# Kernel optimization log

Hardware: AMD Instinct MI355X
Metric: run time of the kernel (lower is better)

The kernel has to match this reference:

```python
import jax, jax.numpy as jnp
import numpy as np

B = 2; L = 5000; C_IN = 12
D_MODEL = 512; D_STATE = 64; D_CONV = 4
D_INNER = 2 * D_MODEL            # mamba expand=2
DT_RANK = (D_MODEL + 15) // 16   # ceil(d_model/16) = 32
NUM_CLASSES = 8


def setup_inputs() -> dict:
    ks = jax.random.split(jax.random.key(0), 16)
    f32 = jnp.float32
    n = lambda k, s, sc: jax.random.normal(k, s, f32) * sc
    return {
        "x": jax.random.normal(ks[0], (B, C_IN, L), f32),
        # 1x1 convs stored as (out_ch, in_ch)
        "w_init": n(ks[1], (D_MODEL, C_IN), 0.1),
        "w_final": n(ks[2], (C_IN, D_MODEL), 0.05),
        # Mamba params
        "w_in": n(ks[3], (2 * D_INNER, D_MODEL), 0.02),
        "conv_w": n(ks[4], (D_INNER, D_CONV), 0.2),   # depthwise taps
        "conv_b": jnp.zeros((D_INNER,), f32),
        "w_xproj": n(ks[5], (DT_RANK + 2 * D_STATE, D_INNER), 0.02),
        "w_dt": n(ks[6], (D_INNER, DT_RANK), 0.1),
        "b_dt": jnp.full((D_INNER,), -4.6, f32),      # softplus(-4.6) ~ 0.01
        "A_log": jnp.log(jnp.broadcast_to(jnp.arange(1, D_STATE + 1, dtype=f32), (D_INNER, D_STATE))),
        "D": jnp.ones((D_INNER,), f32),
        "w_out": n(ks[7], (D_MODEL, D_INNER), 0.02),
        # MLP head
        "w_fc1": n(ks[8], (512, C_IN * L), 0.004),
        "b_fc1": jnp.zeros((512,), f32),
        "w_fc2": n(ks[9], (256, 512), 0.04),
        "b_fc2": jnp.zeros((256,), f32),
        "w_fc3": n(ks[10], (64, 256), 0.06),
        "b_fc3": jnp.zeros((64,), f32),
        "w_fc4": n(ks[11], (NUM_CLASSES, 64), 0.1),
        "b_fc4": jnp.zeros((NUM_CLASSES,), f32),
    }


def _mamba(u, w_in, conv_w, conv_b, w_xproj, w_dt, b_dt, A_log, D, w_out):
    # u: (B, L, d_model)
    xz = jnp.einsum('bld,ed->ble', u, w_in)            # (B, L, 2*d_inner)
    xi, z = jnp.split(xz, 2, axis=-1)
    # causal depthwise conv, kernel width D_CONV (torch pads d_conv-1, takes [:L])
    xpad = jnp.pad(xi, ((0, 0), (D_CONV - 1, 0), (0, 0)))
    xc = conv_b + sum(xpad[:, k:k + L, :] * conv_w[:, k] for k in range(D_CONV))
    xc = jax.nn.silu(xc)                               # (B, L, d_inner)
    x_dbl = jnp.einsum('bld,ed->ble', xc, w_xproj)
    dt_lo = x_dbl[..., :DT_RANK]
    Bm = x_dbl[..., DT_RANK:DT_RANK + D_STATE]         # (B, L, d_state)
    Cm = x_dbl[..., DT_RANK + D_STATE:]                # (B, L, d_state)
    dt = jax.nn.softplus(jnp.einsum('blr,dr->bld', dt_lo, w_dt) + b_dt)
    A = -jnp.exp(A_log)                                # (d_inner, d_state)

    def step(h, inp):
        dt_t, B_t, C_t, u_t = inp                      # (B,di) (B,ds) (B,ds) (B,di)
        dA = jnp.exp(dt_t[:, :, None] * A)             # (B, d_inner, d_state)
        h = dA * h + (dt_t * u_t)[:, :, None] * B_t[:, None, :]
        y_t = jnp.einsum('bds,bs->bd', h, C_t)
        return h, y_t

    h0 = jnp.zeros((u.shape[0], D_INNER, D_STATE), u.dtype)
    xs = (dt.transpose(1, 0, 2), Bm.transpose(1, 0, 2),
          Cm.transpose(1, 0, 2), xc.transpose(1, 0, 2))
    _, ys = jax.lax.scan(jax.checkpoint(step), h0, xs)  # ys: (L, B, d_inner)
    y = ys.transpose(1, 0, 2) + xc * D
    y = y * jax.nn.silu(z)
    return jnp.einsum('bld,md->blm', y, w_out)          # (B, L, d_model)


def reference(x, w_init, w_final, w_in, conv_w, conv_b, w_xproj, w_dt, b_dt,
              A_log, D, w_out, w_fc1, b_fc1, w_fc2, b_fc2, w_fc3, b_fc3,
              w_fc4, b_fc4):
    # initial 1x1 conv + transpose -> (B, L, d_model)
    h = jnp.einsum('bcl,dc->bld', x, w_init)
    m = _mamba(h, w_in, conv_w, conv_b, w_xproj, w_dt, b_dt, A_log, D, w_out)
    m = jax.nn.selu(m)                                  # AlphaDropout: identity in eval
    o = jnp.einsum('bld,cd->bcl', m, w_final)           # final 1x1 conv -> (B, 12, L)
    f = o.reshape(o.shape[0], -1)                       # (B, 60000)
    f = f @ w_fc1.T + b_fc1
    f = f @ w_fc2.T + b_fc2
    f = f @ w_fc3.T + b_fc3
    return f @ w_fc4.T + b_fc4                          # (B, num_classes)
```

## Files before the change

### kernel.cpp

```cpp
#include <hip/hip_runtime.h>

#define BB 2
#define LL 5000
#define DM 512
#define DI 1024
#define DSz 64
#define DRr 32
#define NXx 160
#define ML (BB*LL)
#define NC 25
#define LC 200

typedef short bf16x8 __attribute__((ext_vector_type(8)));
typedef float f32x4 __attribute__((ext_vector_type(4)));

__device__ __forceinline__ float siluf(float x) { return x / (1.0f + __expf(-x)); }
__device__ __forceinline__ float softplusf(float x) { return fmaxf(x, 0.0f) + log1pf(__expf(-fabsf(x))); }
__device__ __forceinline__ float seluf(float x) {
  const float sc = 1.0507009873554805f, al = 1.6732632423543772f;
  return x > 0.0f ? sc * x : sc * al * (__expf(x) - 1.0f);
}
__device__ __forceinline__ void bfsplit(float v, ushort& hi, ushort& lo) {
  unsigned u = __float_as_uint(v);
  unsigned h = (u + 0x7fffu + ((u >> 16) & 1u)) >> 16;
  hi = (ushort)h;
  float l = v - __uint_as_float(h << 16);
  unsigned ul = __float_as_uint(l);
  lo = (ushort)((ul + 0x7fffu + ((ul >> 16) & 1u)) >> 16);
}
__device__ __forceinline__ float bfrecon(ushort hi, ushort lo) {
  return __uint_as_float((unsigned)hi << 16) + __uint_as_float((unsigned)lo << 16);
}

__global__ __launch_bounds__(256) void cvt_split_kernel(
    const float* __restrict__ src, ushort* __restrict__ hi, ushort* __restrict__ lo, int n)
{
  int i = (blockIdx.x * 256 + threadIdx.x) * 4;
  if (i >= n) return;
  float4 v = *reinterpret_cast<const float4*>(src + i);
  ushort h0, l0, h1, l1, h2, l2, h3, l3;
  bfsplit(v.x, h0, l0); bfsplit(v.y, h1, l1);
  bfsplit(v.z, h2, l2); bfsplit(v.w, h3, l3);
  *reinterpret_cast<ushort4*>(hi + i) = make_ushort4(h0, h1, h2, h3);
  *reinterpret_cast<ushort4*>(lo + i) = make_ushort4(l0, l1, l2, l3);
}

__global__ __launch_bounds__(512) void init_h_split_kernel(
    const float* __restrict__ x, const float* __restrict__ w_init,
    ushort* __restrict__ hh, ushort* __restrict__ hl)
{
  int il = blockIdx.x;
  int b = il / LL, l = il - b * LL;
  int dd = threadIdx.x;
  const float* xp = x + (size_t)b * 12 * LL + l;
  float acc = 0.f;
#pragma unroll
  for (int c = 0; c < 12; ++c) acc = fmaf(xp[(size_t)c * LL], w_init[dd * 12 + c], acc);
  ushort h, lo; bfsplit(acc, h, lo);
  hh[(size_t)il * DM + dd] = h;
  hl[(size_t)il * DM + dd] = lo;
}

template<int ACT, int SPLITN>
__global__ __launch_bounds__(256) void gemm_mfma(
    const ushort* __restrict__ Ahi, const ushort* __restrict__ Alo,
    const ushort* __restrict__ Bhi, const ushort* __restrict__ Blo,
    float* __restrict__ C, float* __restrict__ C2, int M, int N, int K)
{
  __shared__ ushort lds[4][128][40];
  int tid = threadIdx.x;
  int i0 = blockIdx.x * 128, j0 = blockIdx.y * 128;
  int l = tid & 63, wid = tid >> 6;
  int wm = (wid >> 1) * 64, wn = (wid & 1) * 64;
  int lr = l & 15, lk = (l >> 4) * 8;
  int sr = tid >> 1, kb = (tid & 1) * 16;

  f32x4 acc[4][4];
#pragma unroll
  for (int m = 0; m < 4; ++m)
#pragma unroll
    for (int n = 0; n < 4; ++n) acc[m][n] = (f32x4){0.f, 0.f, 0.f, 0.f};

  const uint4 z4 = make_uint4(0u, 0u, 0u, 0u);
  for (int k0 = 0; k0 < K; k0 += 32) {
    __syncthreads();
    {
      int gi = i0 + sr, gj = j0 + sr;
      size_t aoff = (size_t)gi * K + k0 + kb;
      size_t boff = (size_t)gj * K + k0 + kb;
      uint4 a0 = z4, a1 = z4, b0 = z4, b1 = z4, c0 = z4, c1 = z4, d0 = z4, d1 = z4;
      if (gi < M) {
        a0 = *reinterpret_cast<const uint4*>(Ahi + aoff);
        a1 = *reinterpret_cast<const uint4*>(Ahi + aoff + 8);
        b0 = *reinterpret_cast<const uint4*>(Alo + aoff);
        b1 = *reinterpret_cast<const uint4*>(Alo + aoff + 8);
      }
      if (gj < N) {
        c0 = *reinterpret_cast<const uint4*>(Bhi + boff);
        c1 = *reinterpret_cast<const uint4*>(Bhi + boff + 8);
        d0 = *reinterpret_cast<const uint4*>(Blo + boff);
        d1 = *reinterpret_cast<const uint4*>(Blo + boff + 8);
      }
      *reinterpret_cast<uint4*>(&lds[0][sr][kb]) = a0;
      *reinterpret_cast<uint4*>(&lds[0][sr][kb + 8]) = a1;
      *reinterpret_cast<uint4*>(&lds[1][sr][kb]) = b0;
      *reinterpret_cast<uint4*>(&lds[1][sr][kb + 8]) = b1;
      *reinterpret_cast<uint4*>(&lds[2][sr][kb]) = c0;
      *reinterpret_cast<uint4*>(&lds[2][sr][kb + 8]) = c1;
      *reinterpret_cast<uint4*>(&lds[3][sr][kb]) = d0;
      *reinterpret_cast<uint4*>(&lds[3][sr][kb + 8]) = d1;
    }
    __syncthreads();
    bf16x8 ah[4], av[4], bh[4], bv[4];
#pragma unroll
    for (int m = 0; m < 4; ++m) {
      ah[m] = *reinterpret_cast<const bf16x8*>(&lds[0][wm + m * 16 + lr][lk]);
      av[m] = *reinterpret_cast<const bf16x8*>(&lds[1][wm + m * 16 + lr][lk]);
    }
#pragma unroll
    for (int n = 0; n < 4; ++n) {
      bh[n] = *reinterpret_cast<const bf16x8*>(&lds[2][wn + n * 16 + lr][lk]);
      bv[n] = *reinterpret_cast<const bf16x8*>(&lds[3][wn + n * 16 + lr][lk]);
    }
#pragma unroll
    for (int m = 0; m < 4; ++m)
#pragma unroll
      for (int n = 0; n < 4; ++n) {
        acc[m][n] = __builtin_amdgcn_mfma_f32_16x16x32_bf16(ah[m], bh[n], acc[m][n], 0, 0, 0);
        acc[m][n] = __builtin_amdgcn_mfma_f32_16x16x32_bf16(av[m], bh[n], acc[m][n], 0, 0, 0);
        acc[m][n] = __builtin_amdgcn_mfma_f32_16x16x32_bf16(ah[m], bv[n], acc[m][n], 0, 0, 0);
      }
  }

#pragma unroll
  for (int m = 0; m < 4; ++m) {
    int r0 = i0 + wm + m * 16 + (l >> 4) * 4;
#pragma unroll
    for (int n = 0; n < 4; ++n) {
      int gc = j0 + wn + n * 16 + lr;
      if (gc >= N) continue;
#pragma unroll
      for (int q = 0; q < 4; ++q) {
        int gi = r0 + q;
        if (gi >= M) continue;
        float r = acc[m][n][q];
        if (ACT == 1) r = seluf(r);
        if (SPLITN) {
          int half = N >> 1;
          if (gc < half) C[(size_t)gi * half + gc] = r;
          else C2[(size_t)gi * half + (gc - half)] = r;
        } else {
          C[(size_t)gi * N + gc] = r;
        }
      }
    }
  }
}

template<int ACT>
__global__ __launch_bounds__(256) void gemm_nt(
    const float* __restrict__ A, const float* __restrict__ Bw,
    const float* __restrict__ bias, float* __restrict__ C,
    int M, int N, int K, int lda, int ldb)
{
  __shared__ float As[16][132];
  __shared__ float Bs[16][132];
  int tid = threadIdx.x;
  int i0 = blockIdx.x * 128, j0 = blockIdx.y * 128;
  int tx = tid & 15, ty = tid >> 4;
  int lr = tid >> 2, lc = tid & 3;
  float acc[8][8];
#pragma unroll
  for (int u = 0; u < 8; ++u)
#pragma unroll
    for (int v = 0; v < 8; ++v) acc[u][v] = 0.f;

  for (int k0 = 0; k0 < K; k0 += 16) {
    __syncthreads();
#pragma unroll
    for (int hh = 0; hh < 2; ++hh) {
      int row = lr + 64 * hh;
      int gi = i0 + row;
      float4 va = make_float4(0.f, 0.f, 0.f, 0.f);
      if (gi < M) va = *reinterpret_cast<const float4*>(A + (size_t)gi * lda + k0 + lc * 4);
      As[lc * 4 + 0][row] = va.x; As[lc * 4 + 1][row] = va.y;
      As[lc * 4 + 2][row] = va.z; As[lc * 4 + 3][row] = va.w;
      int gj = j0 + row;
      float4 vb = make_float4(0.f, 0.f, 0.f, 0.f);
      if (gj < N) vb = *reinterpret_cast<const float4*>(Bw + (size_t)gj * ldb + k0 + lc * 4);
      Bs[lc * 4 + 0][row] = vb.x; Bs[lc * 4 + 1][row] = vb.y;
      Bs[lc * 4 + 2][row] = vb.z; Bs[lc * 4 + 3][row] = vb.w;
    }
    __syncthreads();
#pragma unroll
    for (int kk = 0; kk < 16; ++kk) {
      float4 a0 = *reinterpret_cast<const float4*>(&As[kk][8 * ty]);
      float4 a1 = *reinterpret_cast<const float4*>(&As[kk][8 * ty + 4]);
      float4 b0 = *reinterpret_cast<const float4*>(&Bs[kk][8 * tx]);
      float4 b1 = *reinterpret_cast<const float4*>(&Bs[kk][8 * tx + 4]);
      float av[8] = {a0.x, a0.y, a0.z, a0.w, a1.x, a1.y, a1.z, a1.w};
      float bv[8] = {b0.x, b0.y, b0.z, b0.w, b1.x, b1.y, b1.z, b1.w};
#pragma unroll
      for (int u = 0; u < 8; ++u)
#pragma unroll
        for (int v = 0; v < 8; ++v) acc[u][v] = fmaf(av[u], bv[v], acc[u][v]);
    }
  }

#pragma unroll
  for (int u = 0; u < 8; ++u) {
    int gi = i0 + 8 * ty + u;
    if (gi >= M) continue;
#pragma unroll
    for (int v = 0; v < 8; ++v) {
      int gj = j0 + 8 * tx + v;
      if (gj >= N) continue;
      float r = acc[u][v];
      if (bias) r += bias[gj];
      if (ACT == 1) r = seluf(r);
      if (ACT == 2) r = softplusf(r);
      C[(size_t)gi * N + gj] = r;
    }
  }
}

__global__ __launch_bounds__(256) void conv_silu_split_kernel(
    const float* __restrict__ xi, const float* __restrict__ cw,
    const float* __restrict__ cb, ushort* __restrict__ xch, ushort* __restrict__ xcl)
{
  int il = blockIdx.x;
  int l = il % LL;
  int d = blockIdx.y * 256 + threadIdx.x;
  float acc = cb[d];
  if (l >= 3) acc = fmaf(xi[(size_t)(il - 3) * DI + d], cw[d * 4 + 0], acc);
  if (l >= 2) acc = fmaf(xi[(size_t)(il - 2) * DI + d], cw[d * 4 + 1], acc);
  if (l >= 1) acc = fmaf(xi[(size_t)(il - 1) * DI + d], cw[d * 4 + 2], acc);
  acc = fmaf(xi[(size_t)il * DI + d], cw[d * 4 + 3], acc);
  float v = siluf(acc);
  ushort h, lo; bfsplit(v, h, lo);
  xch[(size_t)il * DI + d] = h;
  xcl[(size_t)il * DI + d] = lo;
}

template<int ACT>
__global__ __launch_bounds__(256) void transpose_k(
    const float* __restrict__ in, float* __restrict__ out,
    int R, int Cc, int ldin, long long bstr)
{
  __shared__ float tile[32][33];
  const float* ip = in + (size_t)blockIdx.z * bstr;
  float* op = out + (size_t)blockIdx.z * bstr;
  int r0 = blockIdx.x * 32, c0 = blockIdx.y * 32;
  int tx = threadIdx.x, ty2 = threadIdx.y;
#pragma unroll
  for (int i = ty2; i < 32; i += 8) {
    int r = r0 + i, c = c0 + tx;
    if (r < R && c < Cc) {
      float v = ip[(size_t)r * ldin + c];
      if (ACT == 1) v = siluf(v);
      tile[i][tx] = v;
    }
  }
  __syncthreads();
#pragma unroll
  for (int i = ty2; i < 32; i += 8) {
    int c = c0 + i, r = r0 + tx;
    if (r < R && c < Cc) op[(size_t)c * R + r] = tile[tx][i];
  }
}

__global__ __launch_bounds__(256) void transpose_recon_k(
    const ushort* __restrict__ inhi, const ushort* __restrict__ inlo,
    float* __restrict__ out, int R, int Cc, int ldin, long long bstr)
{
  __shared__ float tile[32][33];
  const ushort* iph = inhi + (size_t)blockIdx.z * bstr;
  const ushort* ipl = inlo + (size_t)blockIdx.z * bstr;
  float* op = out + (size_t)blockIdx.z * bstr;
  int r0 = blockIdx.x * 32, c0 = blockIdx.y * 32;
  int tx = threadIdx.x, ty2 = threadIdx.y;
#pragma unroll
  for (int i = ty2; i < 32; i += 8) {
    int r = r0 + i, c = c0 + tx;
    if (r < R && c < Cc) {
      size_t idx = (size_t)r * ldin + c;
      tile[i][tx] = bfrecon(iph[idx], ipl[idx]);
    }
  }
  __syncthreads();
#pragma unroll
  for (int i = ty2; i < 32; i += 8) {
    int c = c0 + i, r = r0 + tx;
    if (r < R && c < Cc) op[(size_t)c * R + r] = tile[tx][i];
  }
}

__global__ __launch_bounds__(256) void transpose_split_k(
    const float* __restrict__ in, ushort* __restrict__ outhi, ushort* __restrict__ outlo,
    int R, int Cc, int ldin, long long bstr)
{
  __shared__ float tile[32][33];
  const float* ip = in + (size_t)blockIdx.z * bstr;
  ushort* oph = outhi + (size_t)blockIdx.z * bstr;
  ushort* opl = outlo + (size_t)blockIdx.z * bstr;
  int r0 = blockIdx.x * 32, c0 = blockIdx.y * 32;
  int tx = threadIdx.x, ty2 = threadIdx.y;
#pragma unroll
  for (int i = ty2; i < 32; i += 8) {
    int r = r0 + i, c = c0 + tx;
    if (r < R && c < Cc) tile[i][tx] = ip[(size_t)r * ldin + c];
  }
  __syncthreads();
#pragma unroll
  for (int i = ty2; i < 32; i += 8) {
    int c = c0 + i, r = r0 + tx;
    if (r < R && c < Cc) {
      ushort h, lo; bfsplit(tile[tx][i], h, lo);
      size_t idx = (size_t)c * R + r;
      oph[idx] = h; opl[idx] = lo;
    }
  }
}

__global__ __launch_bounds__(256) void scan_part_kernel(
    const float* __restrict__ dtT, const float* __restrict__ uT,
    const float* __restrict__ xdbl, const float* __restrict__ A_log,
    float2* __restrict__ part)
{
  int task = (blockIdx.x * 256 + threadIdx.x) >> 4;
  int j = threadIdx.x & 15;
  int bd = task / NC, c = task - bd * NC;
  int b = bd >> 10, d = bd & (DI - 1);
  float4 Al = *reinterpret_cast<const float4*>(A_log + d * DSz + 4 * j);
  float Ac0 = -__expf(Al.x), Ac1 = -__expf(Al.y), Ac2 = -__expf(Al.z), Ac3 = -__expf(Al.w);
  size_t base = (size_t)bd * LL + c * LC;
  const float* pdt = dtT + base;
  const float* pu = uT + base;
  const float4* pB4 = reinterpret_cast<const float4*>(
      xdbl + ((size_t)b * LL + c * LC) * NXx + DRr) + j;
  float h0 = 0.f, h1 = 0.f, h2 = 0.f, h3 = 0.f;
  float ap0 = 1.f, ap1 = 1.f, ap2 = 1.f, ap3 = 1.f;
#pragma unroll 4
  for (int t = 0; t < LC; ++t) {
    float dtv = pdt[t];
    float u = pu[t];
    float4 Bv = pB4[0]; pB4 += NXx / 4;
    float du = dtv * u;
    float a0 = __expf(dtv * Ac0); h0 = fmaf(a0, h0, du * Bv.x); ap0 *= a0;
    float a1 = __expf(dtv * Ac1); h1 = fmaf(a1, h1, du * Bv.y); ap1 *= a1;
    float a2 = __expf(dtv * Ac2); h2 = fmaf(a2, h2, du * Bv.z); ap2 *= a2;
    float a3 = __expf(dtv * Ac3); h3 = fmaf(a3, h3, du * Bv.w); ap3 *= a3;
  }
  float4* pw = reinterpret_cast<float4*>(part + (size_t)task * DSz + 4 * j);
  pw[0] = make_float4(ap0, h0, ap1, h1);
  pw[1] = make_float4(ap2, h2, ap3, h3);
}

__global__ __launch_bounds__(256) void scan_y_kernel(
    const float* __restrict__ dtT, const float* __restrict__ uT,
    const float* __restrict__ szT, const float* __restrict__ xdbl,
    const float* __restrict__ A_log, const float* __restrict__ Dv,
    const float2* __restrict__ part, float* __restrict__ yT)
{
  int task = (blockIdx.x * 256 + threadIdx.x) >> 4;
  int j = threadIdx.x & 15;
  int bd = task / NC, c = task - bd * NC;
  int b = bd >> 10, d = bd & (DI - 1);
  float4 Al = *reinterpret_cast<const float4*>(A_log + d * DSz + 4 * j);
  float Ac0 = -__expf(Al.x), Ac1 = -__expf(Al.y), Ac2 = -__expf(Al.z), Ac3 = -__expf(Al.w);
  float Dd = Dv[d];

  float h0 = 0.f, h1 = 0.f, h2 = 0.f, h3 = 0.f;
  const float4* pp = reinterpret_cast<const float4*>(part + (size_t)bd * NC * DSz) + 2 * j;
  for (int p = 0; p < c; ++p) {
    float4 v01 = pp[(size_t)p * (DSz / 2)];
    float4 v23 = pp[(size_t)p * (DSz / 2) + 1];
    h0 = fmaf(v01.x, h0, v01.y);
    h1 = fmaf(v01.z, h1, v01.w);
    h2 = fmaf(v23.x, h2, v23.y);
    h3 = fmaf(v23.z, h3, v23.w);
  }

  size_t base = (size_t)bd * LL + c * LC;
  const float* pdt = dtT + base;
  const float* pu = uT + base;
  const float* psz = szT + base;
  float* py = yT + base;
  const float4* pB4 = reinterpret_cast<const float4*>(
      xdbl + ((size_t)b * LL + c * LC) * NXx + DRr) + j;

  for (int t0 = 0; t0 < LC; t0 += 8) {
    float pr[8], uu[8], szv[8];
#pragma unroll
    for (int i = 0; i < 8; ++i) {
      float dtv = pdt[t0 + i];
      float u = pu[t0 + i];
      uu[i] = u;
      szv[i] = psz[t0 + i];
      float4 Bv = pB4[0];
      float4 Cv = pB4[DSz / 4];
      pB4 += NXx / 4;
      float du = dtv * u;
      float a0 = __expf(dtv * Ac0); h0 = fmaf(a0, h0, du * Bv.x);
      float a1 = __expf(dtv * Ac1); h1 = fmaf(a1, h1, du * Bv.y);
      float a2 = __expf(dtv * Ac2); h2 = fmaf(a2, h2, du * Bv.z);
      float a3 = __expf(dtv * Ac3); h3 = fmaf(a3, h3, du * Bv.w);
      float p = h0 * Cv.x;
      p = fmaf(h1, Cv.y, p);
      p = fmaf(h2, Cv.z, p);
      p = fmaf(h3, Cv.w, p);
      pr[i] = p;
    }
#pragma unroll
    for (int mm = 8; mm >= 1; mm >>= 1) {
#pragma unroll
      for (int i = 0; i < 8; ++i) pr[i] += __shfl_xor(pr[i], mm, 64);
    }
    if (j == 0) {
#pragma unroll
      for (int i = 0; i < 8; ++i) py[t0 + i] = fmaf(uu[i], Dd, pr[i]) * szv[i];
    }
  }
}

__global__ __launch_bounds__(256) void out_proj_kernel(
    const float* __restrict__ m, const float* __restrict__ wf, float* __restrict__ o)
{
  int row = blockIdx.x * 4 + (threadIdx.x >> 6);
  int lane = threadIdx.x & 63;
  int b = row / LL, l = row - b * LL;
  const float* mp = m + (size_t)row * DM;
  float p[12];
#pragma unroll
  for (int c = 0; c < 12; ++c) p[c] = 0.f;
  for (int j0 = 0; j0 < DM; j0 += 64) {
    float mv = mp[j0 + lane];
#pragma unroll
    for (int c = 0; c < 12; ++c) p[c] = fmaf(mv, wf[c * DM + j0 + lane], p[c]);
  }
#pragma unroll
  for (int c = 0; c < 12; ++c) {
    float v = p[c];
#pragma unroll
    for (int mm = 32; mm >= 1; mm >>= 1) v += __shfl_xor(v, mm, 64);
    if (lane == 0) o[(size_t)b * 60000 + c * LL + l] = v;
  }
}

__global__ __launch_bounds__(256) void fc1_kernel(
    const float* __restrict__ o, const float* __restrict__ w1,
    const float* __restrict__ b1, float* __restrict__ f1)
{
  int i = blockIdx.x;
  int tid = threadIdx.x;
  const float* wr = w1 + (size_t)i * 60000;
  float a0 = 0.f, a1 = 0.f;
  for (int idx = tid; idx < 60000; idx += 256) {
    float w = wr[idx];
    a0 = fmaf(o[idx], w, a0);
    a1 = fmaf(o[60000 + idx], w, a1);
  }
#pragma unroll
  for (int mm = 32; mm >= 1; mm >>= 1) { a0 += __shfl_xor(a0, mm, 64); a1 += __shfl_xor(a1, mm, 64); }
  __shared__ float r0[4], r1[4];
  int w4 = tid >> 6;
  if ((tid & 63) == 0) { r0[w4] = a0; r1[w4] = a1; }
  __syncthreads();
  if (tid == 0) {
    f1[i] = r0[0] + r0[1] + r0[2] + r0[3] + b1[i];
    f1[512 + i] = r1[0] + r1[1] + r1[2] + r1[3] + b1[i];
  }
}

__global__ __launch_bounds__(64) void fc2_kernel(
    const float* __restrict__ f1, const float* __restrict__ w2,
    const float* __restrict__ b2, float* __restrict__ f2)
{
  int i = blockIdx.x;
  int lane = threadIdx.x;
  const float* wr = w2 + (size_t)i * 512;
  float a0 = 0.f, a1 = 0.f;
  for (int k = lane; k < 512; k += 64) {
    float w = wr[k];
    a0 = fmaf(f1[k], w, a0);
    a1 = fmaf(f1[512 + k], w, a1);
  }
#pragma unroll
  for (int mm = 32; mm >= 1; mm >>= 1) { a0 += __shfl_xor(a0, mm, 64); a1 += __shfl_xor(a1, mm, 64); }
  if (lane == 0) { f2[i] = a0 + b2[i]; f2[256 + i] = a1 + b2[i]; }
}

__global__ __launch_bounds__(64) void fc34_kernel(
    const float* __restrict__ f2, const float* __restrict__ w3, const float* __restrict__ b3,
    const float* __restrict__ w4, const float* __restrict__ b4, float* __restrict__ outp)
{
  __shared__ float f3[128];
  int t = threadIdx.x;
  float a0 = 0.f, a1 = 0.f;
  for (int k = 0; k < 256; ++k) {
    float w = w3[t * 256 + k];
    a0 = fmaf(f2[k], w, a0);
    a1 = fmaf(f2[256 + k], w, a1);
  }
  f3[t] = a0 + b3[t];
  f3[64 + t] = a1 + b3[t];
  __syncthreads();
  if (t < 16) {
    int b = t >> 3, i = t & 7;
    float a = b4[i];
    for (int k = 0; k < 64; ++k) a = fmaf(f3[b * 64 + k], w4[i * 64 + k], a);
    outp[b * 8 + i] = a;
  }
}

extern "C" void kernel_launch(void* const* d_in, const int* in_sizes, int n_in,
                              void* d_out, int out_size, void* d_ws, size_t ws_size,
                              hipStream_t stream)
{
  const float* x       = (const float*)d_in[0];
  const float* w_init  = (const float*)d_in[1];
  const float* w_final = (const float*)d_in[2];
  const float* w_in    = (const float*)d_in[3];
  const float* conv_w  = (const float*)d_in[4];
  const float* conv_b  = (const float*)d_in[5];
  const float* w_xproj = (const float*)d_in[6];
  const float* w_dt    = (const float*)d_in[7];
  const float* b_dt    = (const float*)d_in[8];
  const float* A_log   = (const float*)d_in[9];
  const float* Dv      = (const float*)d_in[10];
  const float* w_out   = (const float*)d_in[11];
  const float* w_fc1   = (const float*)d_in[12];
  const float* b_fc1   = (const float*)d_in[13];
  const float* w_fc2   = (const float*)d_in[14];
  const float* b_fc2   = (const float*)d_in[15];
  const float* w_fc3   = (const float*)d_in[16];
  const float* b_fc3   = (const float*)d_in[17];
  const float* w_fc4   = (const float*)d_in[18];
  const float* b_fc4   = (const float*)d_in[19];

  float* ws = (float*)d_ws;
  const size_t S7 = 0;
  const size_t S1 = S7 + (size_t)ML * DM;
  const size_t S2 = S1 + (size_t)ML * DI;
  const size_t S3 = S2 + (size_t)ML * DI;
  const size_t S4 = S3 + (size_t)ML * DI;
  const size_t S5 = S4 + (size_t)ML * DI;
  const size_t S8 = S5 + (size_t)ML * DI;
  const size_t S9 = S8 + (size_t)ML * NXx;
  const size_t SF1 = S9 + 120000;
  const size_t SF2 = SF1 + 1024;

  ushort* h_hi = (ushort*)(ws + S7);
  ushort* h_lo = h_hi + (size_t)ML * DM;
  float*  xi   = ws + S1;
  float*  z    = ws + S2;
  ushort* xc_hi = (ushort*)(ws + S3);
  ushort* xc_lo = xc_hi + (size_t)ML * DI;
  float*  dtT  = ws + S4;
  float*  xcT  = ws + S5;
  float*  xdbl = ws + S8;
  float*  dt_l = ws + S1;
  float*  szT  = ws + S3;
  float2* part = (float2*)(ws + S2);
  float*  yT   = ws + S1;
  ushort* y_hi = (ushort*)(ws + S2);
  ushort* y_lo = y_hi + (size_t)ML * DI;
  float*  mbuf = ws + S7;
  float*  o    = ws + S9;
  float*  f1   = ws + SF1;
  float*  f2   = ws + SF2;

  ushort* wb    = (ushort*)(ws + S5);
  ushort* wi_hi = wb;
  ushort* wi_lo = wb + (size_t)2048 * 512;
  ushort* wx_hi = wb + (size_t)2 * 2048 * 512;
  ushort* wx_lo = wx_hi + (size_t)160 * 1024;
  ushort* wo_hi = wb;
  ushort* wo_lo = wb + (size_t)512 * 1024;

  const int GM = (ML + 127) / 128;
  dim3 tb(32, 8);

  cvt_split_kernel<<<1024, 256, 0, stream>>>(w_in, wi_hi, wi_lo, 2048 * 512);
  cvt_split_kernel<<<160, 256, 0, stream>>>(w_xproj, wx_hi, wx_lo, 160 * 1024);
  init_h_split_kernel<<<ML, 512, 0, stream>>>(x, w_init, h_hi, h_lo);
  gemm_mfma<0, 1><<<dim3(GM, 16), 256, 0, stream>>>(h_hi, h_lo, wi_hi, wi_lo, xi, z, ML, 2048, 512);
  conv_silu_split_kernel<<<dim3(ML, DI / 256), 256, 0, stream>>>(xi, conv_w, conv_b, xc_hi, xc_lo);
  gemm_mfma<0, 0><<<dim3(GM, 2), 256, 0, stream>>>(xc_hi, xc_lo, wx_hi, wx_lo, xdbl, nullptr, ML, NXx, 1024);
  gemm_nt<2><<<dim3(GM, DI / 128), 256, 0, stream>>>(xdbl, w_dt, b_dt, dt_l, ML, DI, DRr, NXx, DRr);
  transpose_k<0><<<dim3(157, 32, 2), tb, 0, stream>>>(dt_l, dtT, LL, DI, DI, (long long)LL * DI);
  transpose_recon_k<<<dim3(157, 32, 2), tb, 0, stream>>>(xc_hi, xc_lo, xcT, LL, DI, DI, (long long)LL * DI);
  transpose_k<1><<<dim3(157, 32, 2), tb, 0, stream>>>(z, szT, LL, DI, DI, (long long)LL * DI);
  scan_part_kernel<<<(BB * DI * NC) / 16, 256, 0, stream>>>(dtT, xcT, xdbl, A_log, part);
  scan_y_kernel<<<(BB * DI * NC) / 16, 256, 0, stream>>>(dtT, xcT, szT, xdbl, A_log, Dv, part, yT);
  cvt_split_kernel<<<512, 256, 0, stream>>>(w_out, wo_hi, wo_lo, 512 * 1024);
  transpose_split_k<<<dim3(32, 157, 2), tb, 0, stream>>>(yT, y_hi, y_lo, DI, LL, LL, (long long)LL * DI);
  gemm_mfma<1, 0><<<dim3(GM, 4), 256, 0, stream>>>(y_hi, y_lo, wo_hi, wo_lo, mbuf, nullptr, ML, DM, 1024);
  out_proj_kernel<<<ML / 4, 256, 0, stream>>>(mbuf, w_final, o);
  fc1_kernel<<<512, 256, 0, stream>>>(o, w_fc1, b_fc1, f1);
  fc2_kernel<<<256, 64, 0, stream>>>(f1, w_fc2, b_fc2, f2);
  fc34_kernel<<<1, 64, 0, stream>>>(f2, w_fc3, b_fc3, w_fc4, b_fc4, (float*)d_out);
}
```

Measured before the change: 1.251 ms.

## Fuse transposes into conv and dt-projection kernels, vectorize scan loads

```diff
diff --git a/kernel.cpp b/kernel.cpp
--- a/kernel.cpp
+++ b/kernel.cpp
@@ -27,9 +27,6 @@
   float l = v - __uint_as_float(h << 16);
   unsigned ul = __float_as_uint(l);
   lo = (ushort)((ul + 0x7fffu + ((ul >> 16) & 1u)) >> 16);
-}
-__device__ __forceinline__ float bfrecon(ushort hi, ushort lo) {
-  return __uint_as_float((unsigned)hi << 16) + __uint_as_float((unsigned)lo << 16);
 }
 
 __global__ __launch_bounds__(256) void cvt_split_kernel(
@@ -157,89 +154,76 @@
   }
 }
 
-template<int ACT>
-__global__ __launch_bounds__(256) void gemm_nt(
-    const float* __restrict__ A, const float* __restrict__ Bw,
-    const float* __restrict__ bias, float* __restrict__ C,
-    int M, int N, int K, int lda, int ldb)
-{
-  __shared__ float As[16][132];
-  __shared__ float Bs[16][132];
+__global__ __launch_bounds__(256) void conv_silu_split_t_kernel(
+    const float* __restrict__ xi, const float* __restrict__ cw,
+    const float* __restrict__ cb, ushort* __restrict__ xch, ushort* __restrict__ xcl,
+    float* __restrict__ xcT)
+{
+  __shared__ float tile[32][33];
+  int bz = blockIdx.z;
+  int l0 = blockIdx.x * 32, d0 = blockIdx.y * 32;
+  int tx = threadIdx.x, ty = threadIdx.y;
+  int d = d0 + tx;
+  float c0 = cw[d * 4 + 0], c1 = cw[d * 4 + 1], c2 = cw[d * 4 + 2], c3 = cw[d * 4 + 3];
+  float cbv = cb[d];
+#pragma unroll
+  for (int i = ty; i < 32; i += 8) {
+    int l = l0 + i;
+    if (l < LL) {
+      size_t il = (size_t)bz * LL + l;
+      float acc = cbv;
+      if (l >= 3) acc = fmaf(xi[(il - 3) * DI + d], c0, acc);
+      if (l >= 2) acc = fmaf(xi[(il - 2) * DI + d], c1, acc);
+      if (l >= 1) acc = fmaf(xi[(il - 1) * DI + d], c2, acc);
+      acc = fmaf(xi[il * DI + d], c3, acc);
+      float v = siluf(acc);
+      ushort h, lo; bfsplit(v, h, lo);
+      xch[il * DI + d] = h;
+      xcl[il * DI + d] = lo;
+      tile[i][tx] = v;
+    }
+  }
+  __syncthreads();
+#pragma unroll
+  for (int i = ty; i < 32; i += 8) {
+    int dd = d0 + i, l = l0 + tx;
+    if (l < LL) xcT[((size_t)bz * DI + dd) * LL + l] = tile[tx][i];
+  }
+}
+
+__global__ __launch_bounds__(256) void dtproj_t_kernel(
+    const float* __restrict__ xdbl, const float* __restrict__ w_dt,
+    const float* __restrict__ b_dt, float* __restrict__ dtT)
+{
+  __shared__ float wlds[16][32];
+  __shared__ float blds[16];
+  int bz = blockIdx.z;
+  int l0 = blockIdx.x * 64, d0 = blockIdx.y * 16;
   int tid = threadIdx.x;
-  int i0 = blockIdx.x * 128, j0 = blockIdx.y * 128;
-  int tx = tid & 15, ty = tid >> 4;
-  int lr = tid >> 2, lc = tid & 3;
-  float acc[8][8];
-#pragma unroll
-  for (int u = 0; u < 8; ++u)
-#pragma unroll
-    for (int v = 0; v < 8; ++v) acc[u][v] = 0.f;
-
-  for (int k0 = 0; k0 < K; k0 += 16) {
-    __syncthreads();
-#pragma unroll
-    for (int hh = 0; hh < 2; ++hh) {
-      int row = lr + 64 * hh;
-      int gi = i0 + row;
-      float4 va = make_float4(0.f, 0.f, 0.f, 0.f);
-      if (gi < M) va = *reinterpret_cast<const float4*>(A + (size_t)gi * lda + k0 + lc * 4);
-      As[lc * 4 + 0][row] = va.x; As[lc * 4 + 1][row] = va.y;
-      As[lc * 4 + 2][row] = va.z; As[lc * 4 + 3][row] = va.w;
-      int gj = j0 + row;
-      float4 vb = make_float4(0.f, 0.f, 0.f, 0.f);
-      if (gj < N) vb = *reinterpret_cast<const float4*>(Bw + (size_t)gj * ldb + k0 + lc * 4);
-      Bs[lc * 4 + 0][row] = vb.x; Bs[lc * 4 + 1][row] = vb.y;
-      Bs[lc * 4 + 2][row] = vb.z; Bs[lc * 4 + 3][row] = vb.w;
-    }
-    __syncthreads();
-#pragma unroll
-    for (int kk = 0; kk < 16; ++kk) {
-      float4 a0 = *reinterpret_cast<const float4*>(&As[kk][8 * ty]);
-      float4 a1 = *reinterpret_cast<const float4*>(&As[kk][8 * ty + 4]);
-      float4 b0 = *reinterpret_cast<const float4*>(&Bs[kk][8 * tx]);
-      float4 b1 = *reinterpret_cast<const float4*>(&Bs[kk][8 * tx + 4]);
-      float av[8] = {a0.x, a0.y, a0.z, a0.w, a1.x, a1.y, a1.z, a1.w};
-      float bv[8] = {b0.x, b0.y, b0.z, b0.w, b1.x, b1.y, b1.z, b1.w};
-#pragma unroll
-      for (int u = 0; u < 8; ++u)
-#pragma unroll
-        for (int v = 0; v < 8; ++v) acc[u][v] = fmaf(av[u], bv[v], acc[u][v]);
-    }
-  }
-
-#pragma unroll
-  for (int u = 0; u < 8; ++u) {
-    int gi = i0 + 8 * ty + u;
-    if (gi >= M) continue;
-#pragma unroll
-    for (int v = 0; v < 8; ++v) {
-      int gj = j0 + 8 * tx + v;
-      if (gj >= N) continue;
-      float r = acc[u][v];
-      if (bias) r += bias[gj];
-      if (ACT == 1) r = seluf(r);
-      if (ACT == 2) r = softplusf(r);
-      C[(size_t)gi * N + gj] = r;
-    }
-  }
-}
-
-__global__ __launch_bounds__(256) void conv_silu_split_kernel(
-    const float* __restrict__ xi, const float* __restrict__ cw,
-    const float* __restrict__ cb, ushort* __restrict__ xch, ushort* __restrict__ xcl)
-{
-  int il = blockIdx.x;
-  int l = il % LL;
-  int d = blockIdx.y * 256 + threadIdx.x;
-  float acc = cb[d];
-  if (l >= 3) acc = fmaf(xi[(size_t)(il - 3) * DI + d], cw[d * 4 + 0], acc);
-  if (l >= 2) acc = fmaf(xi[(size_t)(il - 2) * DI + d], cw[d * 4 + 1], acc);
-  if (l >= 1) acc = fmaf(xi[(size_t)(il - 1) * DI + d], cw[d * 4 + 2], acc);
-  acc = fmaf(xi[(size_t)il * DI + d], cw[d * 4 + 3], acc);
-  float v = siluf(acc);
-  ushort h, lo; bfsplit(v, h, lo);
-  xch[(size_t)il * DI + d] = h;
-  xcl[(size_t)il * DI + d] = lo;
+  for (int idx = tid; idx < 512; idx += 256) {
+    int r = idx >> 5, cc = idx & 31;
+    wlds[r][cc] = w_dt[(size_t)(d0 + r) * DRr + cc];
+  }
+  if (tid < 16) blds[tid] = b_dt[d0 + tid];
+  __syncthreads();
+  int lx = tid & 63, ty = tid >> 6;
+  int l = l0 + lx;
+  if (l >= LL) return;
+  const float* xr = xdbl + ((size_t)bz * LL + l) * NXx;
+  float xv[32];
+#pragma unroll
+  for (int q = 0; q < 8; ++q) {
+    float4 v = *reinterpret_cast<const float4*>(xr + 4 * q);
+    xv[4 * q] = v.x; xv[4 * q + 1] = v.y; xv[4 * q + 2] = v.z; xv[4 * q + 3] = v.w;
+  }
+#pragma unroll
+  for (int k = 0; k < 4; ++k) {
+    int dd = ty * 4 + k;
+    float acc = blds[dd];
+#pragma unroll
+    for (int kk = 0; kk < 32; ++kk) acc = fmaf(xv[kk], wlds[dd][kk], acc);
+    dtT[((size_t)bz * DI + d0 + dd) * LL + l] = softplusf(acc);
+  }
 }
 
 template<int ACT>
@@ -269,32 +253,6 @@
   }
 }
 
-__global__ __launch_bounds__(256) void transpose_recon_k(
-    const ushort* __restrict__ inhi, const ushort* __restrict__ inlo,
-    float* __restrict__ out, int R, int Cc, int ldin, long long bstr)
-{
-  __shared__ float tile[32][33];
-  const ushort* iph = inhi + (size_t)blockIdx.z * bstr;
-  const ushort* ipl = inlo + (size_t)blockIdx.z * bstr;
-  float* op = out + (size_t)blockIdx.z * bstr;
-  int r0 = blockIdx.x * 32, c0 = blockIdx.y * 32;
-  int tx = threadIdx.x, ty2 = threadIdx.y;
-#pragma unroll
-  for (int i = ty2; i < 32; i += 8) {
-    int r = r0 + i, c = c0 + tx;
-    if (r < R && c < Cc) {
-      size_t idx = (size_t)r * ldin + c;
-      tile[i][tx] = bfrecon(iph[idx], ipl[idx]);
-    }
-  }
-  __syncthreads();
-#pragma unroll
-  for (int i = ty2; i < 32; i += 8) {
-    int c = c0 + i, r = r0 + tx;
-    if (r < R && c < Cc) op[(size_t)c * R + r] = tile[tx][i];
-  }
-}
-
 __global__ __launch_bounds__(256) void transpose_split_k(
     const float* __restrict__ in, ushort* __restrict__ outhi, ushort* __restrict__ outlo,
     int R, int Cc, int ldin, long long bstr)
@@ -322,6 +280,8 @@
   }
 }
 
+#define L2E 1.44269504088896f
+
 __global__ __launch_bounds__(256) void scan_part_kernel(
     const float* __restrict__ dtT, const float* __restrict__ uT,
     const float* __restrict__ xdbl, const float* __restrict__ A_log,
@@ -332,24 +292,30 @@
   int bd = task / NC, c = task - bd * NC;
   int b = bd >> 10, d = bd & (DI - 1);
   float4 Al = *reinterpret_cast<const float4*>(A_log + d * DSz + 4 * j);
-  float Ac0 = -__expf(Al.x), Ac1 = -__expf(Al.y), Ac2 = -__expf(Al.z), Ac3 = -__expf(Al.w);
+  float Ac0 = -__expf(Al.x) * L2E, Ac1 = -__expf(Al.y) * L2E;
+  float Ac2 = -__expf(Al.z) * L2E, Ac3 = -__expf(Al.w) * L2E;
   size_t base = (size_t)bd * LL + c * LC;
-  const float* pdt = dtT + base;
-  const float* pu = uT + base;
+  const float4* pdt4 = reinterpret_cast<const float4*>(dtT + base);
+  const float4* pu4 = reinterpret_cast<const float4*>(uT + base);
   const float4* pB4 = reinterpret_cast<const float4*>(
       xdbl + ((size_t)b * LL + c * LC) * NXx + DRr) + j;
   float h0 = 0.f, h1 = 0.f, h2 = 0.f, h3 = 0.f;
   float ap0 = 1.f, ap1 = 1.f, ap2 = 1.f, ap3 = 1.f;
-#pragma unroll 4
-  for (int t = 0; t < LC; ++t) {
-    float dtv = pdt[t];
-    float u = pu[t];
-    float4 Bv = pB4[0]; pB4 += NXx / 4;
-    float du = dtv * u;
-    float a0 = __expf(dtv * Ac0); h0 = fmaf(a0, h0, du * Bv.x); ap0 *= a0;
-    float a1 = __expf(dtv * Ac1); h1 = fmaf(a1, h1, du * Bv.y); ap1 *= a1;
-    float a2 = __expf(dtv * Ac2); h2 = fmaf(a2, h2, du * Bv.z); ap2 *= a2;
-    float a3 = __expf(dtv * Ac3); h3 = fmaf(a3, h3, du * Bv.w); ap3 *= a3;
+  for (int t0 = 0; t0 < LC; t0 += 4) {
+    float4 dt4 = pdt4[t0 >> 2];
+    float4 u4 = pu4[t0 >> 2];
+    float dts[4] = {dt4.x, dt4.y, dt4.z, dt4.w};
+    float us[4] = {u4.x, u4.y, u4.z, u4.w};
+#pragma unroll
+    for (int i = 0; i < 4; ++i) {
+      float dtv = dts[i], u = us[i];
+      float4 Bv = pB4[0]; pB4 += NXx / 4;
+      float du = dtv * u;
+      float a0 = exp2f(dtv * Ac0); h0 = fmaf(a0, h0, du * Bv.x); ap0 *= a0;
+      float a1 = exp2f(dtv * Ac1); h1 = fmaf(a1, h1, du * Bv.y); ap1 *= a1;
+      float a2 = exp2f(dtv * Ac2); h2 = fmaf(a2, h2, du * Bv.z); ap2 *= a2;
+      float a3 = exp2f(dtv * Ac3); h3 = fmaf(a3, h3, du * Bv.w); ap3 *= a3;
+    }
   }
   float4* pw = reinterpret_cast<float4*>(part + (size_t)task * DSz + 4 * j);
   pw[0] = make_float4(ap0, h0, ap1, h1);
@@ -367,7 +333,8 @@
   int bd = task / NC, c = task - bd * NC;
   int b = bd >> 10, d = bd & (DI - 1);
   float4 Al = *reinterpret_cast<const float4*>(A_log + d * DSz + 4 * j);
-  float Ac0 = -__expf(Al.x), Ac1 = -__expf(Al.y), Ac2 = -__expf(Al.z), Ac3 = -__expf(Al.w);
+  float Ac0 = -__expf(Al.x) * L2E, Ac1 = -__expf(Al.y) * L2E;
+  float Ac2 = -__expf(Al.z) * L2E, Ac3 = -__expf(Al.w) * L2E;
   float Dd = Dv[d];
 
   float h0 = 0.f, h1 = 0.f, h2 = 0.f, h3 = 0.f;
@@ -382,34 +349,33 @@
   }
 
   size_t base = (size_t)bd * LL + c * LC;
-  const float* pdt = dtT + base;
-  const float* pu = uT + base;
-  const float* psz = szT + base;
-  float* py = yT + base;
+  const float4* pdt4 = reinterpret_cast<const float4*>(dtT + base);
+  const float4* pu4 = reinterpret_cast<const float4*>(uT + base);
+  const float4* psz4 = reinterpret_cast<const float4*>(szT + base);
+  float4* py4 = reinterpret_cast<float4*>(yT + base);
   const float4* pB4 = reinterpret_cast<const float4*>(
       xdbl + ((size_t)b * LL + c * LC) * NXx + DRr) + j;
 
   for (int t0 = 0; t0 < LC; t0 += 8) {
-    float pr[8], uu[8], szv[8];
+    float4 dA = pdt4[0], dB = pdt4[1]; pdt4 += 2;
+    float4 uA = pu4[0], uB = pu4[1]; pu4 += 2;
+    float4 sA = psz4[0], sB = psz4[1]; psz4 += 2;
+    float dts[8] = {dA.x, dA.y, dA.z, dA.w, dB.x, dB.y, dB.z, dB.w};
+    float us[8]  = {uA.x, uA.y, uA.z, uA.w, uB.x, uB.y, uB.z, uB.w};
+    float ss[8]  = {sA.x, sA.y, sA.z, sA.w, sB.x, sB.y, sB.z, sB.w};
+    float pr[8];
 #pragma unroll
     for (int i = 0; i < 8; ++i) {
-      float dtv = pdt[t0 + i];
-      float u = pu[t0 + i];
-      uu[i] = u;
-      szv[i] = psz[t0 + i];
+      float dtv = dts[i], u = us[i];
       float4 Bv = pB4[0];
       float4 Cv = pB4[DSz / 4];
       pB4 += NXx / 4;
       float du = dtv * u;
-      float a0 = __expf(dtv * Ac0); h0 = fmaf(a0, h0, du * Bv.x);
-      float a1 = __expf(dtv * Ac1); h1 = fmaf(a1, h1, du * Bv.y);
-      float a2 = __expf(dtv * Ac2); h2 = fmaf(a2, h2, du * Bv.z);
-      float a3 = __expf(dtv * Ac3); h3 = fmaf(a3, h3, du * Bv.w);
-      float p = h0 * Cv.x;
-      p = fmaf(h1, Cv.y, p);
-      p = fmaf(h2, Cv.z, p);
-      p = fmaf(h3, Cv.w, p);
-      pr[i] = p;
+      float a0 = exp2f(dtv * Ac0); h0 = fmaf(a0, h0, du * Bv.x);
+      float a1 = exp2f(dtv * Ac1); h1 = fmaf(a1, h1, du * Bv.y);
+      float a2 = exp2f(dtv * Ac2); h2 = fmaf(a2, h2, du * Bv.z);
+      float a3 = exp2f(dtv * Ac3); h3 = fmaf(a3, h3, du * Bv.w);
+      pr[i] = fmaf(h3, Cv.w, fmaf(h2, Cv.z, fmaf(h1, Cv.y, h0 * Cv.x)));
     }
 #pragma unroll
     for (int mm = 8; mm >= 1; mm >>= 1) {
@@ -417,9 +383,13 @@
       for (int i = 0; i < 8; ++i) pr[i] += __shfl_xor(pr[i], mm, 64);
     }
     if (j == 0) {
-#pragma unroll
-      for (int i = 0; i < 8; ++i) py[t0 + i] = fmaf(uu[i], Dd, pr[i]) * szv[i];
-    }
+      float4 o0 = make_float4(fmaf(us[0], Dd, pr[0]) * ss[0], fmaf(us[1], Dd, pr[1]) * ss[1],
+                              fmaf(us[2], Dd, pr[2]) * ss[2], fmaf(us[3], Dd, pr[3]) * ss[3]);
+      float4 o1 = make_float4(fmaf(us[4], Dd, pr[4]) * ss[4], fmaf(us[5], Dd, pr[5]) * ss[5],
+                              fmaf(us[6], Dd, pr[6]) * ss[6], fmaf(us[7], Dd, pr[7]) * ss[7]);
+      py4[0] = o0; py4[1] = o1;
+    }
+    py4 += 2;
   }
 }
 
@@ -559,7 +529,6 @@
   float*  dtT  = ws + S4;
   float*  xcT  = ws + S5;
   float*  xdbl = ws + S8;
-  float*  dt_l = ws + S1;
   float*  szT  = ws + S3;
   float2* part = (float2*)(ws + S2);
   float*  yT   = ws + S1;
@@ -570,13 +539,13 @@
   float*  f1   = ws + SF1;
   float*  f2   = ws + SF2;
 
-  ushort* wb    = (ushort*)(ws + S5);
+  ushort* wb    = (ushort*)(ws + S4);
   ushort* wi_hi = wb;
   ushort* wi_lo = wb + (size_t)2048 * 512;
   ushort* wx_hi = wb + (size_t)2 * 2048 * 512;
   ushort* wx_lo = wx_hi + (size_t)160 * 1024;
-  ushort* wo_hi = wb;
-  ushort* wo_lo = wb + (size_t)512 * 1024;
+  ushort* wo_hi = (ushort*)(ws + S5);
+  ushort* wo_lo = wo_hi + (size_t)512 * 1024;
 
   const int GM = (ML + 127) / 128;
   dim3 tb(32, 8);
@@ -585,11 +554,9 @@
   cvt_split_kernel<<<160, 256, 0, stream>>>(w_xproj, wx_hi, wx_lo, 160 * 1024);
   init_h_split_kernel<<<ML, 512, 0, stream>>>(x, w_init, h_hi, h_lo);
   gemm_mfma<0, 1><<<dim3(GM, 16), 256, 0, stream>>>(h_hi, h_lo, wi_hi, wi_lo, xi, z, ML, 2048, 512);
-  conv_silu_split_kernel<<<dim3(ML, DI / 256), 256, 0, stream>>>(xi, conv_w, conv_b, xc_hi, xc_lo);
+  conv_silu_split_t_kernel<<<dim3(157, 32, 2), tb, 0, stream>>>(xi, conv_w, conv_b, xc_hi, xc_lo, xcT);
   gemm_mfma<0, 0><<<dim3(GM, 2), 256, 0, stream>>>(xc_hi, xc_lo, wx_hi, wx_lo, xdbl, nullptr, ML, NXx, 1024);
-  gemm_nt<2><<<dim3(GM, DI / 128), 256, 0, stream>>>(xdbl, w_dt, b_dt, dt_l, ML, DI, DRr, NXx, DRr);
-  transpose_k<0><<<dim3(157, 32, 2), tb, 0, stream>>>(dt_l, dtT, LL, DI, DI, (long long)LL * DI);
-  transpose_recon_k<<<dim3(157, 32, 2), tb, 0, stream>>>(xc_hi, xc_lo, xcT, LL, DI, DI, (long long)LL * DI);
+  dtproj_t_kernel<<<dim3(79, 64, 2), 256, 0, stream>>>(xdbl, w_dt, b_dt, dtT);
   transpose_k<1><<<dim3(157, 32, 2), tb, 0, stream>>>(z, szT, LL, DI, DI, (long long)LL * DI);
   scan_part_kernel<<<(BB * DI * NC) / 16, 256, 0, stream>>>(dtT, xcT, xdbl, A_log, part);
   scan_y_kernel<<<(BB * DI * NC) / 16, 256, 0, stream>>>(dtT, xcT, szT, xdbl, A_log, Dv, part, yT);
```

Result: faster. 1.122 ms (-10.3%).
